# Performance work log

Hardware: AMD Instinct MI355X
Metric: run time of the kernel (lower is better)

Reference implementation:

```python
import jax, jax.numpy as jnp
import numpy as np

KSIZE = 3
STRIDE = 1
RATE = 2
SOFTMAX_SCALE = 10.0
ESCAPE = 1e-4


def _same_pad(x, k, s):
    # TF-style 'SAME' padding as used by the torch same_padding helper
    H, W = x.shape[2], x.shape[3]
    oh, ow = -(-H // s), -(-W // s)
    ph = max((oh - 1) * s + k - H, 0)
    pw = max((ow - 1) * s + k - W, 0)
    return jnp.pad(x, ((0, 0), (0, 0), (ph // 2, ph - ph // 2), (pw // 2, pw - pw // 2)))


def _extract_patches(x, k, s):
    # returns [B, L, C, k, k] patches in row-major (H,W) order, like torch unfold
    xp = _same_pad(x, k, s)
    B, C, H, W = xp.shape
    Ho, Wo = (H - k) // s + 1, (W - k) // s + 1
    cols = [xp[:, :, u:u + (Ho - 1) * s + 1:s, v:v + (Wo - 1) * s + 1:s]
            for u in range(k) for v in range(k)]
    p = jnp.stack(cols, axis=-1)                                   # [B,C,Ho,Wo,k*k]
    p = p.transpose(0, 2, 3, 1, 4).reshape(B, Ho * Wo, C, k, k)
    return p, Ho, Wo


def _contextual(b, mask):
    B, C, H, W = b.shape
    kernel = 2 * RATE
    # raw 4x4 patches of full-res b: used as dynamic deconv kernels
    raw_w, Hr, Wr = _extract_patches(b, kernel, RATE * STRIDE)      # [B,L,C,4,4]
    # nearest-neighbor 1/rate downsample (matches F.interpolate nearest)
    f = b[:, :, ::RATE, ::RATE]                                     # [B,C,Hs,Ws]
    m_s = mask[:, :, ::RATE, ::RATE]
    # 3x3 matching patches of downsampled b (here foreground == background)
    w, Hs, Ws = _extract_patches(f, KSIZE, STRIDE)                  # [B,L,C,3,3]
    L = Hs * Ws
    m, _, _ = _extract_patches(m_s, KSIZE, STRIDE)                  # [1,L,1,3,3]
    mm = (jnp.mean(m[0], axis=(1, 2, 3)) == 0.0).astype(b.dtype)[None, :, None]  # [1,L,1]
    # L2-normalize matching patches (escape-NaN clamp)
    norm = jnp.sqrt(jnp.sum(w * w, axis=(2, 3, 4), keepdims=True))
    wn = (w / jnp.maximum(norm, ESCAPE)).reshape(B, L, C * KSIZE * KSIZE)
    xf = w.reshape(B, L, C * KSIZE * KSIZE)  # patches of f (f == downsampled b)
    # per-sample conv2d(f, wn) == batched matmul over flattened patch dims
    yi = jnp.einsum('bpd,bld->blp', xf, wn)                         # [B,L,P], P=Hs*Ws
    yi = yi * mm
    yi = jax.nn.softmax(yi * SOFTMAX_SCALE, axis=1)
    yi = yi * mm
    # per-sample conv_transpose2d(yi, raw_w, stride=rate, padding=1) / 4
    patches = jnp.einsum('blp,bld->bpd', yi, raw_w.reshape(B, L, C * kernel * kernel))
    Pc = patches.reshape(B, Hs, Ws, C, kernel, kernel).transpose(0, 3, 4, 5, 1, 2)  # [B,C,k,k,Hs,Ws]
    pad = 1
    Hp, Wp = (Hs - 1) * RATE + kernel, (Ws - 1) * RATE + kernel
    out = jnp.zeros((B, C, Hp, Wp), b.dtype)
    for u in range(kernel):
        for v in range(kernel):
            out = out.at[:, :, u:u + (Hs - 1) * RATE + 1:RATE,
                         v:v + (Ws - 1) * RATE + 1:RATE].add(Pc[:, :, u, v])
    out = out[:, :, pad:Hp - pad, pad:Wp - pad]                     # [B,C,H,W]
    return out / 4.0


def setup_inputs() -> dict:
    key = jax.random.key(0)
    b = jax.random.normal(key, (4, 64, 80, 80), dtype=jnp.float32)
    mask = jnp.zeros((1, 1, 80, 80), dtype=jnp.float32)
    return {"b": b, "mask": mask}


def reference(b, mask):
    return _contextual(b, mask)
```

## Files before the change

### kernel.cpp

```cpp
#include <hip/hip_runtime.h>
#include <hip/hip_bf16.h>

#define L 1600
#define LP 1664
#define CCH 64
#define H 80
#define W_ 80
#define HS 40
#define KD 576
#define KR 1024
#define NB 4
#define NT1 13
#define NPAIR 91
#define MT2P 8
#define NT2P 25

typedef __hip_bfloat16 bf16;
typedef short bfrag __attribute__((ext_vector_type(8)));
typedef float f32x4 __attribute__((ext_vector_type(4)));
typedef short short4_t __attribute__((ext_vector_type(4)));
typedef short short8_t __attribute__((ext_vector_type(8)));

__device__ __forceinline__ void gload16(const void* g, void* l) {
    __builtin_amdgcn_global_load_lds(
        (const __attribute__((address_space(1))) unsigned int*)g,
        (__attribute__((address_space(3))) unsigned int*)l, 16, 0, 0);
}

__device__ __forceinline__ int xcd_wgid(int orig, int nwg) {
    int q = nwg >> 3, r = nwg & 7;
    int xcd = orig & 7, iw = orig >> 3;
    return (xcd < r) ? xcd * (q + 1) + iw : r * (q + 1) + (xcd - r) * q + iw;
}

__global__ void build_w_kernel(const float* __restrict__ b,
                               bf16* __restrict__ Wm,
                               float* __restrict__ norms) {
    int bl = blockIdx.x;
    int batch = bl / LP, l = bl % LP;
    int t = threadIdx.x;
    if (l >= L) {
        Wm[(size_t)bl * KD + t] = __float2bfloat16(0.f);
        if (t == 0) norms[bl] = 1.f;
        return;
    }
    int lh = l / HS, lw = l % HS;
    int c = t / 9, r = t % 9;
    int i = r / 3, j = r % 3;
    int y = lh + i - 1, x = lw + j - 1;
    float v = 0.f;
    if (y >= 0 && y < HS && x >= 0 && x < HS)
        v = b[((size_t)(batch * CCH + c) * H + 2 * y) * W_ + 2 * x];
    Wm[(size_t)bl * KD + t] = __float2bfloat16(v);

    float s = v * v;
    #pragma unroll
    for (int o = 32; o > 0; o >>= 1) s += __shfl_down(s, o, 64);
    __shared__ float ws[9];
    if ((t & 63) == 0) ws[t >> 6] = s;
    __syncthreads();
    if (t == 0) {
        float tot = 0.f;
        #pragma unroll
        for (int w = 0; w < 9; ++w) tot += ws[w];
        norms[bl] = sqrtf(tot);
    }
}

__global__ void mm_kernel(const float* __restrict__ mask, float* __restrict__ mmv) {
    int l = blockIdx.x * blockDim.x + threadIdx.x;
    if (l >= LP) return;
    if (l >= L) { mmv[l] = 0.f; return; }
    int lh = l / HS, lw = l % HS;
    float s = 0.f;
    for (int i = 0; i < 3; ++i)
        for (int j = 0; j < 3; ++j) {
            int y = lh + i - 1, x = lw + j - 1;
            if (y >= 0 && y < HS && x >= 0 && x < HS)
                s += mask[(2 * y) * W_ + 2 * x];
        }
    mmv[l] = ((s / 9.0f) == 0.0f) ? 1.f : 0.f;
}

__global__ void build_rt_kernel(const float* __restrict__ b, bf16* __restrict__ Rt) {
    int idx = blockIdx.x * 256 + threadIdx.x;
    int lp = idx % (LP / 8);
    int rest = idx / (LP / 8);
    int d = rest % KR, batch = rest / KR;
    int l8 = lp * 8;
    short8_t pack = {};
    if (l8 < L) {
        int c = d >> 4, u = (d >> 2) & 3, v = d & 3;
        int lh = l8 / HS, lw0 = l8 % HS;
        int y = 2 * lh + u - 1;
        if (y >= 0 && y < H) {
            const float* row = b + ((size_t)(batch * CCH + c) * H + y) * W_;
            #pragma unroll
            for (int j = 0; j < 8; ++j) {
                int x = 2 * (lw0 + j) + v - 1;
                float val = (x >= 0 && x < W_) ? row[x] : 0.f;
                bf16 hv = __float2bfloat16(val);
                pack[j] = *reinterpret_cast<short*>(&hv);
            }
        }
    }
    *reinterpret_cast<short8_t*>(Rt + ((size_t)batch * KR + d) * LP + l8) = pack;
}

template<int ROWS>
__device__ __forceinline__ void stage_tile(const char* gbase, size_t strideB,
                                           char* lds, int wave, int lane) {
    #pragma unroll
    for (int it = 0; it < ROWS / 32; ++it) {
        int cb = it * 256 + wave * 64;
        int c = cb + lane;
        int row = c >> 3, s = c & 7;
        const char* g = gbase + (size_t)row * strideB + ((s ^ (row & 7)) << 4);
        gload16(g, lds + (size_t)cb * 16);
    }
}

__global__ __launch_bounds__(256) void gemm1_kernel(
    const bf16* __restrict__ Wm, const float* __restrict__ norms,
    const float* __restrict__ mmv, bf16* __restrict__ E, float* __restrict__ Sp) {
    __shared__ __align__(128) bf16 smem[2 * 128 * 64];
    __shared__ float Ssh[2][128];
    __shared__ float Ssh2[2][128];
    bf16* As = smem;
    bf16* Bs = smem + 128 * 64;
    bf16* T  = smem;
    int tid = threadIdx.x, lane = tid & 63, wave = tid >> 6;
    int wm = wave >> 1, wn = wave & 1;
    const int nwg = NB * NPAIR;
    int wgid = xcd_wgid(blockIdx.x, nwg);
    int batch = wgid / NPAIR;
    int t91 = wgid % NPAIR;
    int m = 0;
    while (t91 >= NT1 - m) { t91 -= NT1 - m; ++m; }
    int n = m + t91;
    bool diag = (m == n);
    int m0 = m * 128, n0 = n * 128;

    const char* Ag = (const char*)(Wm + ((size_t)batch * LP + m0) * KD);
    const char* Bg = (const char*)(Wm + ((size_t)batch * LP + n0) * KD);
    const size_t sKD = (size_t)KD * 2;

    f32x4 acc[4][4] = {};
    for (int k0 = 0; k0 < KD; k0 += 64) {
        stage_tile<128>(Ag + (size_t)k0 * 2, sKD, (char*)As, wave, lane);
        stage_tile<128>(Bg + (size_t)k0 * 2, sKD, (char*)Bs, wave, lane);
        __syncthreads();
        #pragma unroll
        for (int h = 0; h < 2; ++h) {
            bfrag af[4], bfv[4];
            #pragma unroll
            for (int mi = 0; mi < 4; ++mi) {
                int r = wm * 64 + mi * 16 + (lane & 15);
                int sl = (h * 4 + (lane >> 4)) ^ (r & 7);
                af[mi] = *(const bfrag*)((const char*)As + r * 128 + sl * 16);
            }
            #pragma unroll
            for (int nj = 0; nj < 4; ++nj) {
                int r = wn * 64 + nj * 16 + (lane & 15);
                int sl = (h * 4 + (lane >> 4)) ^ (r & 7);
                bfv[nj] = *(const bfrag*)((const char*)Bs + r * 128 + sl * 16);
            }
            #pragma unroll
            for (int mi = 0; mi < 4; ++mi)
                #pragma unroll
                for (int nj = 0; nj < 4; ++nj)
                    acc[mi][nj] = __builtin_amdgcn_mfma_f32_16x16x32_bf16(
                        af[mi], bfv[nj], acc[mi][nj], 0, 0, 0);
        }
        __syncthreads();
    }

    const float* nr = norms + (size_t)batch * LP;
    bf16* Eb = E + (size_t)batch * LP * LP;

    float Mp[4][4], scp[4][4], mmp[4][4], vldp[4][4];
    #pragma unroll
    for (int mi = 0; mi < 4; ++mi)
        #pragma unroll
        for (int jj = 0; jj < 4; ++jj) {
            int p = m0 + wm * 64 + mi * 16 + (lane >> 4) * 4 + jj;
            float np = nr[p];
            float mp = mmv[p];
            Mp[mi][jj] = 10.0f * np;
            scp[mi][jj] = 10.0f / fmaxf(np, 1e-4f) * mp;
            mmp[mi][jj] = mp;
            vldp[mi][jj] = (p < L) ? 1.f : 0.f;
        }

    float rs1[4][4] = {};
    float rs2[4] = {};

    #pragma unroll
    for (int nj = 0; nj < 4; ++nj) {
        int l_loc = wn * 64 + nj * 16 + (lane & 15);
        int l = n0 + l_loc;
        float nl = nr[l];
        float mml = mmv[l];
        float scl = 10.0f / fmaxf(nl, 1e-4f) * mml;
        float Ml = 10.0f * nl;
        float vldl = (l < L) ? 1.f : 0.f;
        #pragma unroll
        for (int mi = 0; mi < 4; ++mi) {
            short4_t pk = {};
            int p_base = wm * 64 + mi * 16 + (lane >> 4) * 4;
            #pragma unroll
            for (int jj = 0; jj < 4; ++jj) {
                float dotv = acc[mi][nj][jj];
                int p = m0 + p_base + jj;
                float e1 = __expf(dotv * scl - Mp[mi][jj]);
                rs1[mi][jj] += e1 * vldl;
                Eb[(size_t)p * LP + l] = __float2bfloat16(e1 * mml);
                if (!diag) {
                    float e2 = __expf(dotv * scp[mi][jj] - Ml);
                    rs2[nj] += e2 * vldp[mi][jj];
                    bf16 hv = __float2bfloat16(e2 * mmp[mi][jj]);
                    pk[jj] = *reinterpret_cast<short*>(&hv);
                }
            }
            if (!diag) {
                int sl2 = (p_base >> 3) ^ (l_loc & 7);
                *(short4_t*)((char*)T + l_loc * 256 + sl2 * 16 + (p_base & 7) * 2) = pk;
            }
        }
    }

    #pragma unroll
    for (int mi = 0; mi < 4; ++mi)
        #pragma unroll
        for (int jj = 0; jj < 4; ++jj) {
            float v = rs1[mi][jj];
            v += __shfl_xor(v, 1, 64);
            v += __shfl_xor(v, 2, 64);
            v += __shfl_xor(v, 4, 64);
            v += __shfl_xor(v, 8, 64);
            if ((lane & 15) == 0)
                Ssh[wn][wm * 64 + mi * 16 + (lane >> 4) * 4 + jj] = v;
        }
    if (!diag) {
        #pragma unroll
        for (int nj = 0; nj < 4; ++nj) {
            float v = rs2[nj];
            v += __shfl_xor(v, 16, 64);
            v += __shfl_xor(v, 32, 64);
            if (lane < 16) Ssh2[wm][wn * 64 + nj * 16 + lane] = v;
        }
    }
    __syncthreads();
    if (tid < 128) {
        Sp[(size_t)n * (NB * LP) + (size_t)batch * LP + m0 + tid] =
            Ssh[0][tid] + Ssh[1][tid];
        if (!diag)
            Sp[(size_t)m * (NB * LP) + (size_t)batch * LP + n0 + tid] =
                Ssh2[0][tid] + Ssh2[1][tid];
    }
    if (!diag) {
        #pragma unroll
        for (int it = 0; it < 8; ++it) {
            int c = it * 256 + tid;
            int row = c >> 4, col16 = c & 15;
            int slot = col16 ^ (row & 7);
            short8_t v = *(const short8_t*)((const char*)T + row * 256 + slot * 16);
            *(short8_t*)(Eb + (size_t)(n0 + row) * LP + m0 + col16 * 8) = v;
        }
    }
}

__global__ __launch_bounds__(256) void gemm2_kernel(
    const bf16* __restrict__ E, const bf16* __restrict__ Rt,
    const float* __restrict__ Sp, bf16* __restrict__ P2t) {
    __shared__ __align__(128) bf16 As[128 * 64];
    __shared__ __align__(128) bf16 Bs[64 * 64];
    __shared__ float invS[64];
    __shared__ int ntflag[NT1];
    int tid = threadIdx.x, lane = tid & 63, wave = tid >> 6;
    int wm = wave >> 1, wn = wave & 1;
    const int nwg = NB * NT2P * MT2P;
    int wgid = xcd_wgid(blockIdx.x, nwg);
    int m = wgid % MT2P;
    int n = (wgid / MT2P) % NT2P;
    int batch = wgid / (MT2P * NT2P);
    int m0 = m * 128, n0 = n * 64;

    if (tid < NT1) ntflag[tid] = 0;
    if (tid < 64) {
        float s = 0.f;
        float sv[NT1];
        #pragma unroll
        for (int nt = 0; nt < NT1; ++nt) {
            sv[nt] = Sp[(size_t)nt * (NB * LP) + (size_t)batch * LP + n0 + tid];
            s += sv[nt];
        }
        invS[tid] = 1.0f / s;
        float thr = s * 1e-6f;
        #pragma unroll
        for (int nt = 0; nt < NT1; ++nt)
            if (sv[nt] > thr) atomicOr(&ntflag[nt], 1);
    }
    __syncthreads();

    const char* Ag = (const char*)(Rt + ((size_t)batch * KR + m0) * LP);
    const char* Bg = (const char*)(E + ((size_t)batch * LP + n0) * LP);
    const size_t sLP = (size_t)LP * 2;

    f32x4 acc[4][2] = {};
    for (int k0 = 0; k0 < L; k0 += 64) {
        if (!ntflag[k0 >> 7]) continue;
        stage_tile<128>(Ag + (size_t)k0 * 2, sLP, (char*)As, wave, lane);
        stage_tile<64>(Bg + (size_t)k0 * 2, sLP, (char*)Bs, wave, lane);
        __syncthreads();
        #pragma unroll
        for (int h = 0; h < 2; ++h) {
            bfrag af[4], bfv[2];
            #pragma unroll
            for (int mi = 0; mi < 4; ++mi) {
                int r = wm * 64 + mi * 16 + (lane & 15);
                int sl = (h * 4 + (lane >> 4)) ^ (r & 7);
                af[mi] = *(const bfrag*)((const char*)As + r * 128 + sl * 16);
            }
            #pragma unroll
            for (int nj = 0; nj < 2; ++nj) {
                int r = wn * 32 + nj * 16 + (lane & 15);
                int sl = (h * 4 + (lane >> 4)) ^ (r & 7);
                bfv[nj] = *(const bfrag*)((const char*)Bs + r * 128 + sl * 16);
            }
            #pragma unroll
            for (int mi = 0; mi < 4; ++mi)
                #pragma unroll
                for (int nj = 0; nj < 2; ++nj)
                    acc[mi][nj] = __builtin_amdgcn_mfma_f32_16x16x32_bf16(
                        af[mi], bfv[nj], acc[mi][nj], 0, 0, 0);
        }
        __syncthreads();
    }

    bf16* outb = P2t + (size_t)batch * KR * LP;
    #pragma unroll
    for (int nj = 0; nj < 2; ++nj) {
        int pl = wn * 32 + nj * 16 + (lane & 15);
        float is = invS[pl];
        #pragma unroll
        for (int mi = 0; mi < 4; ++mi)
            #pragma unroll
            for (int jj = 0; jj < 4; ++jj) {
                int d = m0 + wm * 64 + mi * 16 + (lane >> 4) * 4 + jj;
                outb[(size_t)d * LP + n0 + pl] =
                    __float2bfloat16(acc[mi][nj][jj] * is);
            }
    }
}

__global__ void fold_kernel(const bf16* __restrict__ P2t, float* __restrict__ out) {
    size_t idx = (size_t)blockIdx.x * blockDim.x + threadIdx.x;
    if (idx >= (size_t)NB * CCH * H * W_) return;
    int x = (int)(idx % W_);
    int y = (int)((idx / W_) % H);
    int c = (int)((idx / ((size_t)W_ * H)) % CCH);
    int batch = (int)(idx / ((size_t)W_ * H * CCH));
    int yp = y + 1, xp = x + 1;
    float s = 0.f;
    #pragma unroll
    for (int du = 0; du < 2; ++du) {
        int u = (yp & 1) + 2 * du;
        int ph2 = yp - u;
        if (ph2 < 0) continue;
        int ph = ph2 >> 1;
        if (ph >= HS) continue;
        #pragma unroll
        for (int dv = 0; dv < 2; ++dv) {
            int v = (xp & 1) + 2 * dv;
            int pw2 = xp - v;
            if (pw2 < 0) continue;
            int pw = pw2 >> 1;
            if (pw >= HS) continue;
            s += __bfloat162float(
                P2t[((size_t)batch * KR + c * 16 + u * 4 + v) * LP + ph * HS + pw]);
        }
    }
    out[idx] = 0.25f * s;
}

extern "C" void kernel_launch(void* const* d_in, const int* in_sizes, int n_in,
                              void* d_out, int out_size, void* d_ws, size_t ws_size,
                              hipStream_t stream) {
    const float* b    = (const float*)d_in[0];
    const float* mask = (const float*)d_in[1];
    float* out = (float*)d_out;

    char* w = (char*)d_ws;
    bf16* Wb = (bf16*)w;  w += (size_t)NB * LP * KD * 2;
    bf16* Rt = (bf16*)w;  w += (size_t)NB * KR * LP * 2;
    bf16* E  = (bf16*)w;  w += (size_t)NB * LP * LP * 2;
    bf16* P2t = (bf16*)w; w += (size_t)NB * KR * LP * 2;
    float* norms = (float*)w; w += (size_t)NB * LP * 4;
    float* mmv = (float*)w;   w += (size_t)LP * 4;
    float* Sp = (float*)w;    w += (size_t)NT1 * NB * LP * 4;

    build_w_kernel<<<NB * LP, KD, 0, stream>>>(b, Wb, norms);
    mm_kernel<<<(LP + 255) / 256, 256, 0, stream>>>(mask, mmv);
    build_rt_kernel<<<NB * KR * (LP / 8) / 256, 256, 0, stream>>>(b, Rt);

    gemm1_kernel<<<NB * NPAIR, 256, 0, stream>>>(Wb, norms, mmv, E, Sp);
    gemm2_kernel<<<NB * NT2P * MT2P, 256, 0, stream>>>(E, Rt, Sp, P2t);

    fold_kernel<<<(int)(((size_t)NB * CCH * H * W_ + 255) / 256), 256, 0, stream>>>(P2t, out);
}
```

Before: 81.56 us.

## Skip negligible softmax tiles in gemm1 epilogue and fuse mask kernel

Before the exponentials, the gemm1 epilogue computes a block-wide maximum of the shifted logits for each direction of the symmetric tile pair. If that maximum falls below -21, the exp evaluation, the row-sum accumulation and the E stores for that direction are skipped, since those terms are tiny next to the self-match maximum. This is meant to cut the expf work and the large E write traffic for dissimilar tile pairs. In exchange it adds a reduction and a barrier, and it leaves E tiles unwritten, which relies on gemm2 ignoring tiles whose partial sums are zero. The mask-validity kernel is also folded into build_w_kernel to save one launch.

```diff
diff --git a/kernel.cpp b/kernel.cpp
--- a/kernel.cpp
+++ b/kernel.cpp
@@ -35,10 +35,27 @@
 
 __global__ void build_w_kernel(const float* __restrict__ b,
                                bf16* __restrict__ Wm,
-                               float* __restrict__ norms) {
+                               float* __restrict__ norms,
+                               const float* __restrict__ mask,
+                               float* __restrict__ mmv) {
     int bl = blockIdx.x;
     int batch = bl / LP, l = bl % LP;
     int t = threadIdx.x;
+    if (batch == 0 && t == 0) {
+        float mv = 0.f;
+        if (l < L) {
+            int lh = l / HS, lw = l % HS;
+            float s = 0.f;
+            for (int i = 0; i < 3; ++i)
+                for (int j = 0; j < 3; ++j) {
+                    int y = lh + i - 1, x = lw + j - 1;
+                    if (y >= 0 && y < HS && x >= 0 && x < HS)
+                        s += mask[(2 * y) * W_ + 2 * x];
+                }
+            mv = ((s / 9.0f) == 0.0f) ? 1.f : 0.f;
+        }
+        mmv[l] = mv;
+    }
     if (l >= L) {
         Wm[(size_t)bl * KD + t] = __float2bfloat16(0.f);
         if (t == 0) norms[bl] = 1.f;
@@ -65,21 +82,6 @@
         for (int w = 0; w < 9; ++w) tot += ws[w];
         norms[bl] = sqrtf(tot);
     }
-}
-
-__global__ void mm_kernel(const float* __restrict__ mask, float* __restrict__ mmv) {
-    int l = blockIdx.x * blockDim.x + threadIdx.x;
-    if (l >= LP) return;
-    if (l >= L) { mmv[l] = 0.f; return; }
-    int lh = l / HS, lw = l % HS;
-    float s = 0.f;
-    for (int i = 0; i < 3; ++i)
-        for (int j = 0; j < 3; ++j) {
-            int y = lh + i - 1, x = lw + j - 1;
-            if (y >= 0 && y < HS && x >= 0 && x < HS)
-                s += mask[(2 * y) * W_ + 2 * x];
-        }
-    mmv[l] = ((s / 9.0f) == 0.0f) ? 1.f : 0.f;
 }
 
 __global__ void build_rt_kernel(const float* __restrict__ b, bf16* __restrict__ Rt) {
@@ -126,6 +128,7 @@
     __shared__ __align__(128) bf16 smem[2 * 128 * 64];
     __shared__ float Ssh[2][128];
     __shared__ float Ssh2[2][128];
+    __shared__ float mxsh[2][4];
     bf16* As = smem;
     bf16* Bs = smem + 128 * 64;
     bf16* T  = smem;
@@ -191,40 +194,74 @@
             mmp[mi][jj] = mp;
             vldp[mi][jj] = (p < L) ? 1.f : 0.f;
         }
+    float scl_a[4], Ml_a[4], mml_a[4], vldl_a[4];
+    #pragma unroll
+    for (int nj = 0; nj < 4; ++nj) {
+        int l = n0 + wn * 64 + nj * 16 + (lane & 15);
+        float nl = nr[l];
+        float mml = mmv[l];
+        scl_a[nj] = 10.0f / fmaxf(nl, 1e-4f) * mml;
+        Ml_a[nj] = 10.0f * nl;
+        mml_a[nj] = mml;
+        vldl_a[nj] = (l < L) ? 1.f : 0.f;
+    }
+
+    float mx1 = -1e30f, mx2 = -1e30f;
+    #pragma unroll
+    for (int nj = 0; nj < 4; ++nj)
+        #pragma unroll
+        for (int mi = 0; mi < 4; ++mi)
+            #pragma unroll
+            for (int jj = 0; jj < 4; ++jj) {
+                float d = acc[mi][nj][jj];
+                mx1 = fmaxf(mx1, d * scl_a[nj] - Mp[mi][jj]);
+                mx2 = fmaxf(mx2, d * scp[mi][jj] - Ml_a[nj]);
+            }
+    #pragma unroll
+    for (int o = 32; o > 0; o >>= 1) {
+        mx1 = fmaxf(mx1, __shfl_xor(mx1, o, 64));
+        mx2 = fmaxf(mx2, __shfl_xor(mx2, o, 64));
+    }
+    if (lane == 0) { mxsh[0][wave] = mx1; mxsh[1][wave] = mx2; }
+    __syncthreads();
+    bool do1 = fmaxf(fmaxf(mxsh[0][0], mxsh[0][1]), fmaxf(mxsh[0][2], mxsh[0][3])) > -21.0f;
+    bool do2 = !diag &&
+        fmaxf(fmaxf(mxsh[1][0], mxsh[1][1]), fmaxf(mxsh[1][2], mxsh[1][3])) > -21.0f;
 
     float rs1[4][4] = {};
     float rs2[4] = {};
 
-    #pragma unroll
-    for (int nj = 0; nj < 4; ++nj) {
-        int l_loc = wn * 64 + nj * 16 + (lane & 15);
-        int l = n0 + l_loc;
-        float nl = nr[l];
-        float mml = mmv[l];
-        float scl = 10.0f / fmaxf(nl, 1e-4f) * mml;
-        float Ml = 10.0f * nl;
-        float vldl = (l < L) ? 1.f : 0.f;
-        #pragma unroll
-        for (int mi = 0; mi < 4; ++mi) {
-            short4_t pk = {};
-            int p_base = wm * 64 + mi * 16 + (lane >> 4) * 4;
-            #pragma unroll
-            for (int jj = 0; jj < 4; ++jj) {
-                float dotv = acc[mi][nj][jj];
-                int p = m0 + p_base + jj;
-                float e1 = __expf(dotv * scl - Mp[mi][jj]);
-                rs1[mi][jj] += e1 * vldl;
-                Eb[(size_t)p * LP + l] = __float2bfloat16(e1 * mml);
-                if (!diag) {
-                    float e2 = __expf(dotv * scp[mi][jj] - Ml);
-                    rs2[nj] += e2 * vldp[mi][jj];
-                    bf16 hv = __float2bfloat16(e2 * mmp[mi][jj]);
-                    pk[jj] = *reinterpret_cast<short*>(&hv);
+    if (do1 || do2) {
+        #pragma unroll
+        for (int nj = 0; nj < 4; ++nj) {
+            int l_loc = wn * 64 + nj * 16 + (lane & 15);
+            int l = n0 + l_loc;
+            float scl = scl_a[nj], Ml = Ml_a[nj];
+            float mml = mml_a[nj], vldl = vldl_a[nj];
+            #pragma unroll
+            for (int mi = 0; mi < 4; ++mi) {
+                short4_t pk = {};
+                int p_base = wm * 64 + mi * 16 + (lane >> 4) * 4;
+                #pragma unroll
+                for (int jj = 0; jj < 4; ++jj) {
+                    float dotv = acc[mi][nj][jj];
+                    if (do1) {
+                        int p = m0 + p_base + jj;
+                        float e1 = __expf(dotv * scl - Mp[mi][jj]);
+                        rs1[mi][jj] += e1 * vldl;
+                        Eb[(size_t)p * LP + l] = __float2bfloat16(e1 * mml);
+                    }
+                    if (do2) {
+                        float e2 = __expf(dotv * scp[mi][jj] - Ml);
+                        rs2[nj] += e2 * vldp[mi][jj];
+                        bf16 hv = __float2bfloat16(e2 * mmp[mi][jj]);
+                        pk[jj] = *reinterpret_cast<short*>(&hv);
+                    }
                 }
-            }
-            if (!diag) {
-                int sl2 = (p_base >> 3) ^ (l_loc & 7);
-                *(short4_t*)((char*)T + l_loc * 256 + sl2 * 16 + (p_base & 7) * 2) = pk;
+                if (do2) {
+                    int sl2 = (p_base >> 3) ^ (l_loc & 7);
+                    *(short4_t*)((char*)T + l_loc * 256 + sl2 * 16 + (p_base & 7) * 2) = pk;
+                }
             }
         }
     }
@@ -258,7 +295,7 @@
             Sp[(size_t)m * (NB * LP) + (size_t)batch * LP + n0 + tid] =
                 Ssh2[0][tid] + Ssh2[1][tid];
     }
-    if (!diag) {
+    if (do2) {
         #pragma unroll
         for (int it = 0; it < 8; ++it) {
             int c = it * 256 + tid;
@@ -400,8 +437,7 @@
     float* mmv = (float*)w;   w += (size_t)LP * 4;
     float* Sp = (float*)w;    w += (size_t)NT1 * NB * LP * 4;
 
-    build_w_kernel<<<NB * LP, KD, 0, stream>>>(b, Wb, norms);
-    mm_kernel<<<(LP + 255) / 256, 256, 0, stream>>>(mask, mmv);
+    build_w_kernel<<<NB * LP, KD, 0, stream>>>(b, Wb, norms, mask, mmv);
     build_rt_kernel<<<NB * KR * (LP / 8) / 256, 256, 0, stream>>>(b, Rt);
 
     gemm1_kernel<<<NB * NPAIR, 256, 0, stream>>>(Wb, norms, mmv, E, Sp);
```

Result: slower. 88.99 us (+9.1%).
